# Optimization experiments

Hardware: AMD Instinct MI355X
Metric: run time of the kernel (lower is better)

Reference implementation:

```python
import jax, jax.numpy as jnp
import numpy as np

S, B, D = 2048, 2, 2048      # seq, batch, hidden  (x is [S, B, D])
H, KV, HD = 16, 4, 128        # n_head, n_kv_head, head_dim
N_REP = H // KV               # GQA repeat factor
THETA = 10000.0


def setup_inputs() -> dict:
    key = jax.random.key(0)
    ks = jax.random.split(key, 5)
    sc = 1.0 / np.sqrt(D)
    x = jax.random.normal(ks[0], (S, B, D), jnp.float32)
    Wq = jax.random.normal(ks[1], (D, H * HD), jnp.float32) * sc
    Wk = jax.random.normal(ks[2], (D, KV * HD), jnp.float32) * sc
    Wv = jax.random.normal(ks[3], (D, KV * HD), jnp.float32) * sc
    Wo = jax.random.normal(ks[4], (H * HD, D), jnp.float32) * sc
    return {"x": x, "Wq": Wq, "Wk": Wk, "Wv": Wv, "Wo": Wo}


def _rope_cos_sin(seq_len, dim, theta):
    inv_freq = 1.0 / (theta ** (jnp.arange(0, dim, 2, dtype=jnp.float32) / dim))
    t = jnp.arange(seq_len, dtype=jnp.float32)
    freqs = jnp.outer(t, inv_freq)                  # [S, dim/2]
    emb = jnp.concatenate([freqs, freqs], axis=-1)  # [S, dim]
    return jnp.cos(emb), jnp.sin(emb)


def _rotate_half(u):
    u1, u2 = jnp.split(u, 2, axis=-1)
    return jnp.concatenate([-u2, u1], axis=-1)


def reference(x, Wq, Wk, Wv, Wo):
    # projections (torch Linear without bias; W stored as [in, out] here)
    q = (x @ Wq).reshape(S, B, H, HD)
    k = (x @ Wk).reshape(S, B, KV, HD)
    v = (x @ Wv).reshape(S, B, KV, HD)

    # RoPE (full rotary, partial_rotary_factor == 1.0)
    cos, sin = _rope_cos_sin(S, HD, THETA)
    cos = cos[:, None, None, :]  # [S,1,1,HD] broadcasts over B, heads
    sin = sin[:, None, None, :]
    q = q * cos + _rotate_half(q) * sin
    k = k * cos + _rotate_half(k) * sin

    # GQA: repeat_interleave kv heads to match query heads
    k = jnp.repeat(k, N_REP, axis=2)
    v = jnp.repeat(v, N_REP, axis=2)

    # [S,B,H,HD] -> [B,H,S,HD]
    q = q.transpose(1, 2, 0, 3)
    k = k.transpose(1, 2, 0, 3)
    v = v.transpose(1, 2, 0, 3)

    # causal SDPA (dropout_p = 0 in eval)
    scale = 1.0 / np.sqrt(HD)
    scores = jnp.einsum('bhqd,bhkd->bhqk', q, k) * scale
    causal = jnp.tril(jnp.ones((S, S), dtype=bool))
    scores = jnp.where(causal, scores, jnp.finfo(scores.dtype).min)
    probs = jax.nn.softmax(scores, axis=-1)
    out = jnp.einsum('bhqk,bhkd->bhqd', probs, v)

    # [B,H,S,HD] -> [S,B,D], then output projection
    out = out.transpose(2, 0, 1, 3).reshape(S, B, D)
    return out @ Wo
```

## Files before the change

kernel.cpp:

```cpp
#include <hip/hip_runtime.h>
#include <hip/hip_bf16.h>
#include <cstdint>
#include <math.h>

#define S_LEN   2048
#define B_SZ    2
#define D_MODEL 2048
#define NH      16
#define NKV     4
#define HD      128
#define ROWS    (S_LEN * B_SZ)
#define NQKV    3072
#define SCALE   0.08838834764831845f

typedef __attribute__((ext_vector_type(8))) short short8;
typedef __attribute__((ext_vector_type(4))) float f32x4;

__device__ __forceinline__ short f2bf(float f) {
  union { float f; unsigned u; } v; v.f = f;
  unsigned r = v.u + 0x7fffu + ((v.u >> 16) & 1u);
  return (short)(r >> 16);
}
__device__ __forceinline__ float bf2f(short x) {
  union { unsigned u; float f; } v;
  v.u = ((unsigned)(unsigned short)x) << 16;
  return v.f;
}

__device__ __forceinline__ void async16(const short* g, short* l) {
  __builtin_amdgcn_global_load_lds(
      (const __attribute__((address_space(1))) void*)(uintptr_t)(const void*)g,
      (__attribute__((address_space(3))) void*)(uintptr_t)(void*)l,
      16, 0, 0);
}

__global__ void cvt_bf16_kernel(const float* __restrict__ src, short* __restrict__ dst, int n4) {
  int t = blockIdx.x * blockDim.x + threadIdx.x;
  if (t >= n4) return;
  float4 v = ((const float4*)src)[t];
  short4 o;
  o.x = f2bf(v.x); o.y = f2bf(v.y); o.z = f2bf(v.z); o.w = f2bf(v.w);
  *(short4*)(dst + (size_t)t * 4) = o;
}

__global__ void wtrans_qkv_kernel(const float* __restrict__ Wq,
                                  const float* __restrict__ Wk,
                                  const float* __restrict__ Wv,
                                  short* __restrict__ dst) {
  __shared__ float tile[32][33];
  const int bx = blockIdx.x;
  const float* src;
  int Ndim, n0, drow;
  if (bx < 64)      { src = Wq; Ndim = 2048; n0 = bx * 32;        drow = n0; }
  else if (bx < 80) { src = Wk; Ndim = 512;  n0 = (bx - 64) * 32; drow = 2048 + n0; }
  else              { src = Wv; Ndim = 512;  n0 = (bx - 80) * 32; drow = 2560 + n0; }
  const int k0 = blockIdx.y * 32;
  for (int r = threadIdx.y; r < 32; r += 8)
    tile[r][threadIdx.x] = src[(size_t)(k0 + r) * Ndim + n0 + threadIdx.x];
  __syncthreads();
  for (int r = threadIdx.y; r < 32; r += 8)
    dst[(size_t)(drow + r) * 2048 + k0 + threadIdx.x] = f2bf(tile[threadIdx.x][r]);
}

__global__ void wtrans_kernel(const float* __restrict__ src, short* __restrict__ dst,
                              int Kdim, int Ndim) {
  __shared__ float tile[32][33];
  int n0 = blockIdx.x * 32, k0 = blockIdx.y * 32;
  for (int r = threadIdx.y; r < 32; r += 8)
    tile[r][threadIdx.x] = src[(size_t)(k0 + r) * Ndim + n0 + threadIdx.x];
  __syncthreads();
  for (int r = threadIdx.y; r < 32; r += 8)
    dst[(size_t)(n0 + r) * Kdim + k0 + threadIdx.x] = f2bf(tile[threadIdx.x][r]);
}

#define BM 128
#define BN 128
#define BK 32

template<int BF16OUT>
__global__ __launch_bounds__(256) void gemm_bt_kernel(const short* __restrict__ A,
    const short* __restrict__ Bt, void* __restrict__ Cv, int M, int N, int K) {
  __shared__ alignas(16) short As[BM * BK];
  __shared__ alignas(16) short Bs[BN * BK];
  const int tid  = threadIdx.x;
  const int wave = tid >> 6;
  const int lane = tid & 63;
  const int quad = lane >> 4;
  const int lr   = lane & 15;
  const int m0 = blockIdx.y * BM;
  const int n0 = blockIdx.x * BN;
  const int wm = (wave >> 1) * 64;
  const int wn = (wave & 1) * 64;

  f32x4 acc[4][4];
#pragma unroll
  for (int i = 0; i < 4; i++)
#pragma unroll
    for (int j = 0; j < 4; j++) acc[i][j] = (f32x4){0.f, 0.f, 0.f, 0.f};

  const int r0 = tid >> 2,          c0 = (tid & 3) * 8;
  const int r1 = (tid + 256) >> 2,  c1 = (tid & 3) * 8;

  for (int kt = 0; kt < K; kt += BK) {
    const short* ga = A  + (size_t)m0 * K + kt;
    const short* gb = Bt + (size_t)n0 * K + kt;
    async16(ga + (size_t)r0 * K + c0, As + wave * 512);
    async16(ga + (size_t)r1 * K + c1, As + 2048 + wave * 512);
    async16(gb + (size_t)r0 * K + c0, Bs + wave * 512);
    async16(gb + (size_t)r1 * K + c1, Bs + 2048 + wave * 512);
    __syncthreads();

    short8 a[4], b[4];
#pragma unroll
    for (int i = 0; i < 4; i++) a[i] = *(const short8*)(As + (wm + i * 16 + lr) * BK + quad * 8);
#pragma unroll
    for (int j = 0; j < 4; j++) b[j] = *(const short8*)(Bs + (wn + j * 16 + lr) * BK + quad * 8);
#pragma unroll
    for (int i = 0; i < 4; i++)
#pragma unroll
      for (int j = 0; j < 4; j++)
        acc[i][j] = __builtin_amdgcn_mfma_f32_16x16x32_bf16(a[i], b[j], acc[i][j], 0, 0, 0);
    __syncthreads();
  }

#pragma unroll
  for (int i = 0; i < 4; i++) {
    const int row = m0 + wm + i * 16 + quad * 4;
#pragma unroll
    for (int j = 0; j < 4; j++) {
      const int col = n0 + wn + j * 16 + lr;
#pragma unroll
      for (int r = 0; r < 4; r++) {
        float v = acc[i][j][r];
        if (BF16OUT) ((short*)Cv)[(size_t)(row + r) * N + col] = f2bf(v);
        else         ((float*)Cv)[(size_t)(row + r) * N + col] = v;
      }
    }
  }
}

__global__ void rope_kernel(const short* __restrict__ QKVb, short* __restrict__ Qb,
                            short* __restrict__ Kpack) {
  const int head = blockIdx.y;
  const int t = blockIdx.x * blockDim.x + threadIdx.x;
  const int i = t & 63;
  const int row = t >> 6;
  const int s = row >> 1;
  const int b = row & 1;
  float inv_freq = __expf(-(float)i * (1.0f / 64.0f) * 9.210340371976184f);
  float ang = (float)s * inv_freq;
  float sn, cs;
  __sincosf(ang, &sn, &cs);
  if (head < NH) {
    const short* p = QKVb + (size_t)row * NQKV + head * HD;
    float v1 = bf2f(p[i]), v2 = bf2f(p[i + 64]);
    short* q = Qb + ((size_t)(b * NH + head) * S_LEN + s) * HD;
    q[i]      = f2bf((v1 * cs - v2 * sn) * SCALE);
    q[i + 64] = f2bf((v2 * cs + v1 * sn) * SCALE);
  } else {
    const int kv = head - NH;
    const short* p = QKVb + (size_t)row * NQKV + NH * HD + kv * HD;
    float v1 = bf2f(p[i]), v2 = bf2f(p[i + 64]);
    float k1 = v1 * cs - v2 * sn;
    float k2 = v2 * cs + v1 * sn;
    short* kp = Kpack + (size_t)(b * NKV + kv) * S_LEN * HD;
    const int tile = s >> 4, lrr = s & 15;
    const int d1 = i, d2 = i + 64;
    kp[(size_t)((tile * 4 + (d1 >> 5)) * 64 + ((d1 >> 3) & 3) * 16 + lrr) * 8 + (d1 & 7)] = f2bf(k1);
    kp[(size_t)((tile * 4 + (d2 >> 5)) * 64 + ((d2 >> 3) & 3) * 16 + lrr) * 8 + (d2 & 7)] = f2bf(k2);
  }
}

__global__ void vpack_kernel(const short* __restrict__ QKVb, short* __restrict__ Vpack) {
  __shared__ short tile[32][136];
  const int tid = threadIdx.x;
  const int chunk = blockIdx.x & 63, stream = blockIdx.x >> 6;
  const int b = stream >> 2, kv = stream & 3;
  const int vcol = NH * HD + NKV * HD + kv * HD;
  {
    const int r = tid >> 3, c = (tid & 7) * 16;
    const short* src = QKVb + (size_t)((chunk * 32 + r) * B_SZ + b) * NQKV + vcol + c;
    *(short8*)(&tile[r][c])     = *(const short8*)(src);
    *(short8*)(&tile[r][c + 8]) = *(const short8*)(src + 8);
  }
  __syncthreads();
  const int wave = tid >> 6, lane = tid & 63, quad = lane >> 4, lr = lane & 15;
  short* dst = Vpack + (size_t)stream * HD * S_LEN + chunk * 4096 + lane * 8;
#pragma unroll
  for (int k = 0; k < 2; ++k) {
    const int dt = wave + k * 4;
    short8 v;
#pragma unroll
    for (int j = 0; j < 8; ++j) v[j] = tile[quad * 8 + j][dt * 16 + lr];
    *(short8*)(dst + dt * 512) = v;
  }
}

#define PSP 72

template<bool MASK>
__device__ __forceinline__ void attn_iter64(
    const short* __restrict__ Ks, const short* __restrict__ Vs,
    short* __restrict__ Psw, const short8 qf[4], int kv0, int nt, int qlim,
    int quad, int lr, int lane, f32x4 o[8], float& m_i, float& l_i)
{
  const int lane_off = lane * 8;
  f32x4 sc[4];
#pragma unroll
  for (int t = 0; t < 4; ++t) {
    if (t < nt) {
      const short* kp = Ks + t * 2048 + lane_off;
      f32x4 s = (f32x4){0.f, 0.f, 0.f, 0.f};
#pragma unroll
      for (int c = 0; c < 4; ++c) {
        short8 kf = *(const short8*)(kp + c * 512);
        s = __builtin_amdgcn_mfma_f32_16x16x32_bf16(kf, qf[c], s, 0, 0, 0);
      }
      sc[t] = s;
    } else {
      sc[t] = (f32x4){-3.0e38f, -3.0e38f, -3.0e38f, -3.0e38f};
    }
  }
  if (MASK) {
#pragma unroll
    for (int t = 0; t < 4; ++t)
#pragma unroll
      for (int r = 0; r < 4; ++r)
        if (kv0 + t * 16 + quad * 4 + r > qlim) sc[t][r] = -3.0e38f;
  }
  float mb = -3.0e38f;
#pragma unroll
  for (int t = 0; t < 4; ++t)
#pragma unroll
    for (int r = 0; r < 4; ++r) mb = fmaxf(mb, sc[t][r]);
  mb = fmaxf(mb, __shfl_xor(mb, 16, 64));
  mb = fmaxf(mb, __shfl_xor(mb, 32, 64));
  const float mnew = fmaxf(m_i, mb);
  const float alpha = __expf(m_i - mnew);
  m_i = mnew;
  float rs = 0.f;
#pragma unroll
  for (int t = 0; t < 4; ++t) {
    float p0 = __expf(sc[t][0] - mnew);
    float p1 = __expf(sc[t][1] - mnew);
    float p2 = __expf(sc[t][2] - mnew);
    float p3 = __expf(sc[t][3] - mnew);
    rs += (p0 + p1) + (p2 + p3);
    __hip_bfloat162 pk01 = __float22bfloat162_rn(make_float2(p0, p1));
    __hip_bfloat162 pk23 = __float22bfloat162_rn(make_float2(p2, p3));
    __hip_bfloat162* pd = (__hip_bfloat162*)(Psw + lr * PSP + t * 16 + quad * 4);
    pd[0] = pk01;
    pd[1] = pk23;
  }
  rs += __shfl_xor(rs, 16, 64);
  rs += __shfl_xor(rs, 32, 64);
  l_i = l_i * alpha + rs;
#pragma unroll
  for (int n = 0; n < 8; ++n)
#pragma unroll
    for (int r = 0; r < 4; ++r) o[n][r] *= alpha;
  short8 pb0 = *(const short8*)(Psw + lr * PSP + quad * 8);
#pragma unroll
  for (int dt = 0; dt < 8; ++dt) {
    short8 vf = *(const short8*)(Vs + dt * 512 + lane_off);
    o[dt] = __builtin_amdgcn_mfma_f32_16x16x32_bf16(vf, pb0, o[dt], 0, 0, 0);
  }
  if (!MASK || nt > 2) {
    short8 pb1 = *(const short8*)(Psw + lr * PSP + 32 + quad * 8);
#pragma unroll
    for (int dt = 0; dt < 8; ++dt) {
      short8 vf = *(const short8*)(Vs + 4096 + dt * 512 + lane_off);
      o[dt] = __builtin_amdgcn_mfma_f32_16x16x32_bf16(vf, pb1, o[dt], 0, 0, 0);
    }
  }
}

__global__ __launch_bounds__(256) void attn_kernel(const short* __restrict__ Qb,
    const short* __restrict__ Kpack, const short* __restrict__ Vpack,
    short* __restrict__ Ob) {
  __shared__ alignas(16) short Ks[64 * HD];
  __shared__ alignas(16) short Vs[64 * HD];
  __shared__ alignas(16) short Ps[4][16 * PSP];
  const int tid = threadIdx.x, wave = tid >> 6, lane = tid & 63;
  const int quad = lane >> 4, lr = lane & 15;
  const int bid = blockIdx.x;
  const int sid  = bid & 7;
  const int hsub = (bid >> 3) & 3;
  const int qg   = 31 - (bid >> 5);
  const int b = sid >> 2, kvh = sid & 3;
  const int h = kvh * 4 + hsub;
  const int qw = (qg * 4 + wave) * 16;

  const short* Qp  = Qb    + ((size_t)(b * NH + h) * S_LEN + qw) * HD;
  const short* Kpk = Kpack + (size_t)(b * NKV + kvh) * S_LEN * HD;
  const short* Vpk = Vpack + (size_t)(b * NKV + kvh) * HD * S_LEN;
  short* Psw = &Ps[wave][0];

  short8 qf[4];
#pragma unroll
  for (int c = 0; c < 4; ++c)
    qf[c] = *(const short8*)(Qp + lr * HD + c * 32 + quad * 8);

  f32x4 o[8];
#pragma unroll
  for (int n = 0; n < 8; ++n) o[n] = (f32x4){0.f, 0.f, 0.f, 0.f};
  float m_i = -3.0e38f, l_i = 0.f;

  const int qlim = qw + lr;
  for (int it = 0; it <= qg; ++it) {
    const int kv0 = it * 64;
    __syncthreads();
    {
      const short* gk = Kpk + (size_t)kv0 * HD;
      const short* gv = Vpk + (size_t)(kv0 >> 5) * 4096;
#pragma unroll
      for (int k = 0; k < 4; ++k) {
        const int off = (wave * 4 + k) * 512;
        async16(gk + off + lane * 8, Ks + off);
        async16(gv + off + lane * 8, Vs + off);
      }
    }
    __syncthreads();
    if (it < qg)
      attn_iter64<false>(Ks, Vs, Psw, qf, kv0, 4, qlim, quad, lr, lane, o, m_i, l_i);
    else
      attn_iter64<true>(Ks, Vs, Psw, qf, kv0, wave + 1, qlim, quad, lr, lane, o, m_i, l_i);
  }

  const float invl = 1.0f / l_i;
  short* op = Ob + ((size_t)(qw + lr) * B_SZ + b) * D_MODEL + h * HD + quad * 4;
#pragma unroll
  for (int dt = 0; dt < 8; ++dt) {
    short4 ov;
    ov.x = f2bf(o[dt][0] * invl);
    ov.y = f2bf(o[dt][1] * invl);
    ov.z = f2bf(o[dt][2] * invl);
    ov.w = f2bf(o[dt][3] * invl);
    *(short4*)(op + dt * 16) = ov;
  }
}

extern "C" void kernel_launch(void* const* d_in, const int* in_sizes, int n_in,
                              void* d_out, int out_size, void* d_ws, size_t ws_size,
                              hipStream_t stream) {
  (void)in_sizes; (void)n_in; (void)out_size; (void)ws_size;
  const float* x  = (const float*)d_in[0];
  const float* Wq = (const float*)d_in[1];
  const float* Wk = (const float*)d_in[2];
  const float* Wv = (const float*)d_in[3];
  const float* Wo = (const float*)d_in[4];
  float* out = (float*)d_out;
  char* ws = (char*)d_ws;

  short* Wqkv_t = (short*)(ws);
  short* xb     = (short*)(ws + 12582912);
  short* Qb     = (short*)(ws);
  short* Kpack  = (short*)(ws + 16777216);
  short* Vpack  = (short*)(ws + 25165824);
  short* QKVb   = (short*)(ws + 29360128);
  short* Ob     = (short*)(ws + 29360128);
  short* Wo_t   = (short*)(ws + 54525952);

  dim3 tblk(32, 8);

  cvt_bf16_kernel<<<(ROWS * D_MODEL / 4 + 255) / 256, 256, 0, stream>>>(x, xb, ROWS * D_MODEL / 4);
  wtrans_qkv_kernel<<<dim3(96, 64), tblk, 0, stream>>>(Wq, Wk, Wv, Wqkv_t);
  wtrans_kernel<<<dim3(64, 64), tblk, 0, stream>>>(Wo, Wo_t, 2048, 2048);
  gemm_bt_kernel<1><<<dim3(NQKV / BN, ROWS / BM), 256, 0, stream>>>(xb, Wqkv_t, QKVb, ROWS, NQKV, D_MODEL);
  rope_kernel<<<dim3(1024, NH + NKV), 256, 0, stream>>>(QKVb, Qb, Kpack);
  vpack_kernel<<<dim3(512), 256, 0, stream>>>(QKVb, Vpack);
  attn_kernel<<<dim3(1024), 256, 0, stream>>>(Qb, Kpack, Vpack, Ob);
  gemm_bt_kernel<0><<<dim3(D_MODEL / BN, ROWS / BM), 256, 0, stream>>>(Ob, Wo_t, out, ROWS, D_MODEL, D_MODEL);
}
```

Before: 327.3 us.

## Replace GEMM with larger-tile multi-stage pipelined kernel and XCD-aware block swizzle

Replaces the single-buffered 128x128 GEMM with a 512-thread kernel that uses 256-wide N tiles, a 4-slot LDS ring, and three tiles of async global-to-LDS prefetch controlled by explicit vmcnt waits. The kernel also raises MFMA priority with setprio and remaps block ids so neighbouring tiles land on the same chiplet. The goal is to hide global load latency and raise per-block arithmetic intensity for both the QKV and output projections. In exchange it uses much more LDS and more registers per thread, and its correctness rests on hand-counted wait counts.

```diff
diff --git a/kernel.cpp b/kernel.cpp
--- a/kernel.cpp
+++ b/kernel.cpp
@@ -73,65 +73,115 @@
     dst[(size_t)(n0 + r) * Kdim + k0 + threadIdx.x] = f2bf(tile[threadIdx.x][r]);
 }
 
-#define BM 128
-#define BN 128
-#define BK 32
-
-template<int BF16OUT>
-__global__ __launch_bounds__(256) void gemm_bt_kernel(const short* __restrict__ A,
-    const short* __restrict__ Bt, void* __restrict__ Cv, int M, int N, int K) {
-  __shared__ alignas(16) short As[BM * BK];
-  __shared__ alignas(16) short Bs[BN * BK];
+template<int BM, int BF16OUT>
+__global__ __launch_bounds__(512, 2) void gemm2_kernel(const short* __restrict__ A,
+    const short* __restrict__ Bt, void* __restrict__ Cv, int N, int K) {
+  constexpr int MI  = BM / 32;
+  constexpr int PH  = MI / 4;
+  constexpr int APW = BM / 128;
+  constexpr int TC  = APW + 2;
+  constexpr int ASZ = BM * 32;
+  constexpr int BSZ = 256 * 32;
+  constexpr int BUFS = ASZ + BSZ;
+  __shared__ alignas(16) short lds[4 * BUFS];
+
   const int tid  = threadIdx.x;
-  const int wave = tid >> 6;
-  const int lane = tid & 63;
-  const int quad = lane >> 4;
-  const int lr   = lane & 15;
-  const int m0 = blockIdx.y * BM;
-  const int n0 = blockIdx.x * BN;
-  const int wm = (wave >> 1) * 64;
-  const int wn = (wave & 1) * 64;
-
-  f32x4 acc[4][4];
-#pragma unroll
-  for (int i = 0; i < 4; i++)
-#pragma unroll
-    for (int j = 0; j < 4; j++) acc[i][j] = (f32x4){0.f, 0.f, 0.f, 0.f};
-
-  const int r0 = tid >> 2,          c0 = (tid & 3) * 8;
-  const int r1 = (tid + 256) >> 2,  c1 = (tid & 3) * 8;
-
-  for (int kt = 0; kt < K; kt += BK) {
-    const short* ga = A  + (size_t)m0 * K + kt;
-    const short* gb = Bt + (size_t)n0 * K + kt;
-    async16(ga + (size_t)r0 * K + c0, As + wave * 512);
-    async16(ga + (size_t)r1 * K + c1, As + 2048 + wave * 512);
-    async16(gb + (size_t)r0 * K + c0, Bs + wave * 512);
-    async16(gb + (size_t)r1 * K + c1, Bs + 2048 + wave * 512);
-    __syncthreads();
-
-    short8 a[4], b[4];
-#pragma unroll
-    for (int i = 0; i < 4; i++) a[i] = *(const short8*)(As + (wm + i * 16 + lr) * BK + quad * 8);
-#pragma unroll
-    for (int j = 0; j < 4; j++) b[j] = *(const short8*)(Bs + (wn + j * 16 + lr) * BK + quad * 8);
-#pragma unroll
-    for (int i = 0; i < 4; i++)
-#pragma unroll
-      for (int j = 0; j < 4; j++)
-        acc[i][j] = __builtin_amdgcn_mfma_f32_16x16x32_bf16(a[i], b[j], acc[i][j], 0, 0, 0);
-    __syncthreads();
-  }
-
-#pragma unroll
-  for (int i = 0; i < 4; i++) {
-    const int row = m0 + wm + i * 16 + quad * 4;
-#pragma unroll
-    for (int j = 0; j < 4; j++) {
-      const int col = n0 + wn + j * 16 + lr;
-#pragma unroll
-      for (int r = 0; r < 4; r++) {
-        float v = acc[i][j][r];
+  const int w    = tid >> 6, lane = tid & 63;
+  const int quad = lane >> 4, lr = lane & 15;
+  const int wm   = w >> 2, wn = w & 3;
+
+  const int nwg = gridDim.x;
+  const int id  = (blockIdx.x & 7) * (nwg >> 3) + (blockIdx.x >> 3);
+  const int nbx = N >> 8;
+  const int bx = id % nbx, by = id / nbx;
+  const int m0 = by * BM, n0 = bx * 256;
+
+  const short* gA = A  + (size_t)(m0 + w * (16 * APW) + (lane >> 2)) * K + (lane & 3) * 8;
+  const short* gB = Bt + (size_t)(n0 + w * 32 + (lane >> 2)) * K + (lane & 3) * 8;
+
+  const int aoff = (wm * (BM / 2) + lr) * 32 + quad * 8;
+  const int boff = (wn * 64 + lr) * 32 + quad * 8;
+
+  f32x4 acc[MI][4];
+#pragma unroll
+  for (int i = 0; i < MI; ++i)
+#pragma unroll
+    for (int j = 0; j < 4; ++j) acc[i][j] = (f32x4){0.f, 0.f, 0.f, 0.f};
+
+  auto stageA = [&](int t) {
+    short* la = lds + (t & 3) * BUFS;
+    const short* g = gA + t * 32;
+#pragma unroll
+    for (int c = 0; c < APW; ++c)
+      async16(g + (size_t)c * 16 * K, la + (w * APW + c) * 512);
+  };
+  auto stageB = [&](int t) {
+    short* lb = lds + (t & 3) * BUFS + ASZ;
+    const short* g = gB + t * 32;
+#pragma unroll
+    for (int c = 0; c < 2; ++c)
+      async16(g + (size_t)c * 16 * K, lb + (w * 2 + c) * 512);
+  };
+
+  const int NT = K >> 5;
+  stageA(0); stageB(0); stageA(1); stageB(1); stageA(2); stageB(2);
+  asm volatile("s_waitcnt vmcnt(%0)" :: "n"(2 * TC) : "memory");
+  __builtin_amdgcn_s_barrier();
+
+  for (int t = 0; t < NT; ++t) {
+    const short* la = lds + (t & 3) * BUFS;
+    const short* lb = la + ASZ;
+    const bool pre = (t + 3) < NT;
+
+    short8 a0[4], b0[4];
+#pragma unroll
+    for (int j = 0; j < 4; ++j) b0[j] = *(const short8*)(lb + boff + j * 512);
+#pragma unroll
+    for (int i = 0; i < 4; ++i) a0[i] = *(const short8*)(la + aoff + i * 512);
+    if (pre) stageA(t + 3);
+    if (PH == 1 && pre) stageB(t + 3);
+    __builtin_amdgcn_s_barrier();
+    __builtin_amdgcn_s_setprio(1);
+#pragma unroll
+    for (int i = 0; i < 4; ++i)
+#pragma unroll
+      for (int j = 0; j < 4; ++j)
+        acc[i][j] = __builtin_amdgcn_mfma_f32_16x16x32_bf16(a0[i], b0[j], acc[i][j], 0, 0, 0);
+    __builtin_amdgcn_s_setprio(0);
+
+    if (PH == 2) {
+      __builtin_amdgcn_s_barrier();
+      short8 a1[4];
+#pragma unroll
+      for (int i = 0; i < 4; ++i) a1[i] = *(const short8*)(la + aoff + (4 + i) * 512);
+      if (pre) stageB(t + 3);
+      __builtin_amdgcn_s_barrier();
+      __builtin_amdgcn_s_setprio(1);
+#pragma unroll
+      for (int i = 0; i < 4; ++i)
+#pragma unroll
+        for (int j = 0; j < 4; ++j)
+          acc[4 + i][j] = __builtin_amdgcn_mfma_f32_16x16x32_bf16(a1[i], b0[j], acc[4 + i][j], 0, 0, 0);
+      __builtin_amdgcn_s_setprio(0);
+    }
+
+    if (t < NT - 1) {
+      if (t < NT - 3)       asm volatile("s_waitcnt vmcnt(%0)" :: "n"(2 * TC) : "memory");
+      else if (t == NT - 3) asm volatile("s_waitcnt vmcnt(%0)" :: "n"(TC) : "memory");
+      else                  asm volatile("s_waitcnt vmcnt(0)" ::: "memory");
+      __builtin_amdgcn_s_barrier();
+    }
+  }
+
+#pragma unroll
+  for (int i = 0; i < MI; ++i) {
+    const int row = m0 + wm * (BM / 2) + i * 16 + quad * 4;
+#pragma unroll
+    for (int j = 0; j < 4; ++j) {
+      const int col = n0 + wn * 64 + j * 16 + lr;
+#pragma unroll
+      for (int r = 0; r < 4; ++r) {
+        const float v = acc[i][j][r];
         if (BF16OUT) ((short*)Cv)[(size_t)(row + r) * N + col] = f2bf(v);
         else         ((float*)Cv)[(size_t)(row + r) * N + col] = v;
       }
@@ -366,9 +416,9 @@
   cvt_bf16_kernel<<<(ROWS * D_MODEL / 4 + 255) / 256, 256, 0, stream>>>(x, xb, ROWS * D_MODEL / 4);
   wtrans_qkv_kernel<<<dim3(96, 64), tblk, 0, stream>>>(Wq, Wk, Wv, Wqkv_t);
   wtrans_kernel<<<dim3(64, 64), tblk, 0, stream>>>(Wo, Wo_t, 2048, 2048);
-  gemm_bt_kernel<1><<<dim3(NQKV / BN, ROWS / BM), 256, 0, stream>>>(xb, Wqkv_t, QKVb, ROWS, NQKV, D_MODEL);
+  gemm2_kernel<256, 1><<<dim3((NQKV / 256) * (ROWS / 256)), 512, 0, stream>>>(xb, Wqkv_t, QKVb, NQKV, D_MODEL);
   rope_kernel<<<dim3(1024, NH + NKV), 256, 0, stream>>>(QKVb, Qb, Kpack);
   vpack_kernel<<<dim3(512), 256, 0, stream>>>(QKVb, Vpack);
   attn_kernel<<<dim3(1024), 256, 0, stream>>>(Qb, Kpack, Vpack, Ob);
-  gemm_bt_kernel<0><<<dim3(D_MODEL / BN, ROWS / BM), 256, 0, stream>>>(Ob, Wo_t, out, ROWS, D_MODEL, D_MODEL);
-}
+  gemm2_kernel<128, 0><<<dim3((D_MODEL / 256) * (ROWS / 128)), 512, 0, stream>>>(Ob, Wo_t, out, D_MODEL, D_MODEL);
+}
```

After: 314.9 us. 1.04x faster.
